# Performance work log

Hardware: AMD Instinct MI355X
Metric: run time of the kernel (lower is better)

Reference implementation:

```python
import jax, jax.numpy as jnp
import numpy as np

N = 4096
INPUT_DIM = 256
HIDDEN = 64
HEADS = 8
NEG_SLOPE = 0.2
MASK_FILL = -10000.0


def setup_inputs() -> dict:
    key = jax.random.key(0)
    k_x, k_adj, k_w, k_as, k_ad = jax.random.split(key, 5)
    x = jax.random.normal(k_x, (N, INPUT_DIM), dtype=jnp.float32)
    adjacency = jax.random.bernoulli(k_adj, 0.05, (N, N)) | jnp.eye(N, dtype=bool)
    # linear weight, torch convention: [out_features, in_features]
    W = jax.random.normal(k_w, (HEADS * HIDDEN, INPUT_DIM), dtype=jnp.float32) * 0.05
    attn_src = jax.random.normal(k_as, (HEADS, HIDDEN), dtype=jnp.float32) * 0.1
    attn_dst = jax.random.normal(k_ad, (HEADS, HIDDEN), dtype=jnp.float32) * 0.1
    return {"x": x, "adjacency": adjacency, "W": W, "attn_src": attn_src, "attn_dst": attn_dst}


def reference(x, adjacency, W, attn_src, attn_dst):
    # h: [N, heads, hidden]
    h = (x @ W.T).reshape(N, HEADS, HIDDEN)
    src_scores = jnp.einsum('nhd,hd->nh', h, attn_src)  # [N, heads]
    dst_scores = jnp.einsum('nhd,hd->nh', h, attn_dst)  # [N, heads]
    # logits[i, j, h] = src[i, h] + dst[j, h]  (matches torch permute(2,0,1) layout math)
    logits = src_scores[:, None, :] + dst_scores[None, :, :]  # [N, N, heads]
    logits = jax.nn.leaky_relu(logits, negative_slope=NEG_SLOPE)
    logits = jnp.where(adjacency[:, :, None], logits, MASK_FILL)
    alpha = jax.nn.softmax(logits, axis=1)  # softmax over source nodes j
    out = jnp.einsum('ijh,jhf->ihf', alpha, h)  # [N, heads, hidden]
    return out.mean(axis=1)  # [N, hidden]
```

## Files before the change

kernel.cpp:

```cpp
#include <hip/hip_runtime.h>

#define NN 4096
#define IN_DIM 256
#define HID 64
#define HEADS 8

typedef __attribute__((ext_vector_type(4))) float f32x4;
typedef __attribute__((ext_vector_type(8))) short s16x8;
typedef unsigned short u16;
typedef unsigned long long u64;

__device__ inline u16 f2bf(float f) {
  union { float f; unsigned u; } v; v.f = f;
  unsigned r = (v.u + 0x7FFFu + ((v.u >> 16) & 1u)) >> 16;
  return (u16)r;
}
__device__ inline float bf2f(u16 b) {
  union { unsigned u; float f; } v; v.u = ((unsigned)b) << 16;
  return v.f;
}
__device__ __forceinline__ unsigned cvt_pk_bf16(float a, float b) {
  unsigned r;
  asm("v_cvt_pk_bf16_f32 %0, %1, %2" : "=v"(r) : "v"(a), "v"(b));
  return r;
}
__device__ inline unsigned encf(float f) {
  unsigned u = __float_as_uint(f);
  return (u & 0x80000000u) ? ~u : (u | 0x80000000u);
}
__device__ inline float decf(unsigned k) {
  return (k & 0x80000000u) ? __uint_as_float(k & 0x7FFFFFFFu) : __uint_as_float(~k);
}

__global__ __launch_bounds__(256) void gat_prep(
    const void* __restrict__ adj, const float* __restrict__ x,
    const float* __restrict__ W, u64* __restrict__ bits,
    u16* __restrict__ xhi_g, u16* __restrict__ xlo_g,
    u16* __restrict__ whi_g, u16* __restrict__ wlo_g,
    unsigned* __restrict__ Mh_enc)
{
  const int t = threadIdx.x;
  const int gtid = blockIdx.x * 256 + t;
  if (blockIdx.x == 0 && t < 8) Mh_enc[t] = 0u;

  if (gtid < 262144) {
    f32x4 v = ((const f32x4*)x)[gtid];
    ushort4 hi, lo;
    hi.x = f2bf(v[0]); lo.x = f2bf(v[0] - bf2f(hi.x));
    hi.y = f2bf(v[1]); lo.y = f2bf(v[1] - bf2f(hi.y));
    hi.z = f2bf(v[2]); lo.z = f2bf(v[2] - bf2f(hi.z));
    hi.w = f2bf(v[3]); lo.w = f2bf(v[3] - bf2f(hi.w));
    ((ushort4*)xhi_g)[gtid] = hi;
    ((ushort4*)xlo_g)[gtid] = lo;
  }
  if (gtid < 32768) {
    f32x4 v = ((const f32x4*)W)[gtid];
    ushort4 hi, lo;
    hi.x = f2bf(v[0]); lo.x = f2bf(v[0] - bf2f(hi.x));
    hi.y = f2bf(v[1]); lo.y = f2bf(v[1] - bf2f(hi.y));
    hi.z = f2bf(v[2]); lo.z = f2bf(v[2] - bf2f(hi.z));
    hi.w = f2bf(v[3]); lo.w = f2bf(v[3] - bf2f(hi.w));
    ((ushort4*)whi_g)[gtid] = hi;
    ((ushort4*)wlo_g)[gtid] = lo;
  }

  __shared__ int smode;
  if (t < 64) {
    const unsigned char* a8 = (const unsigned char*)adj;
    const int* a32 = (const int*)adj;
    size_t i8 = (size_t)(4 * t + 1) * 4097;
    int p8 = a8[i8] != 0;
    size_t k = (size_t)(2 * t + 1);
    int p32 = a32[k * 4097] != 0;
    int p64 = a32[2 * k * 4097] != 0;
    int ok8 = __all(p8), ok32 = __all(p32), ok64 = __all(p64);
    if (t == 0) smode = ok8 ? 0 : (ok32 ? 1 : (ok64 ? 2 : 1));
  }
  __syncthreads();
  const int mode = smode;

  const int lane = t & 63;
  const int wave = (blockIdx.x * blockDim.x + t) >> 6;
  const int nwaves = (gridDim.x * blockDim.x) >> 6;
  const size_t nwords = (size_t)NN * NN / 64;
  for (size_t w = wave; w < nwords; w += nwaves) {
    size_t e = w * 64 + lane;
    int on;
    if (mode == 1)      on = ((const int*)adj)[e] != 0;
    else if (mode == 0) on = ((const unsigned char*)adj)[e] != 0;
    else                on = ((const long long*)adj)[e] != 0;
    u64 b = __ballot(on);
    if (lane == 0) bits[w] = b;
  }
}

__global__ __launch_bounds__(256) void gat_gemm1(
    const u16* __restrict__ xhi_g, const u16* __restrict__ xlo_g,
    const u16* __restrict__ whi_g, const u16* __restrict__ wlo_g,
    const float* __restrict__ a_src, const float* __restrict__ a_dst,
    u16* __restrict__ Hbt, float* __restrict__ s_srcT,
    float* __restrict__ s_dstT, unsigned* __restrict__ Mh_enc)
{
  __shared__ u16 xhi[64 * 72], xlo[64 * 72], whi[64 * 72], wlo[64 * 72];
  const int nb = blockIdx.x;
  const int ob = blockIdx.y;
  const int t = threadIdx.x;
  const int lane = t & 63, wid = t >> 6;
  const int wr = wid >> 1, wc = wid & 1;
  const int g = lane >> 4;

  f32x4 acc[2][2] = {};

  const int sn = t >> 2;
  const int skc = (t & 3) * 16;

  for (int kb = 0; kb < 4; ++kb) {
    const u16* xh_p = xhi_g + (size_t)(nb * 64 + sn) * IN_DIM + kb * 64 + skc;
    const u16* xl_p = xlo_g + (size_t)(nb * 64 + sn) * IN_DIM + kb * 64 + skc;
    const u16* wh_p = whi_g + (size_t)(ob * 64 + sn) * IN_DIM + kb * 64 + skc;
    const u16* wl_p = wlo_g + (size_t)(ob * 64 + sn) * IN_DIM + kb * 64 + skc;
    const int base = sn * 72 + skc;
    *(s16x8*)(xhi + base)     = *(const s16x8*)(xh_p);
    *(s16x8*)(xhi + base + 8) = *(const s16x8*)(xh_p + 8);
    *(s16x8*)(xlo + base)     = *(const s16x8*)(xl_p);
    *(s16x8*)(xlo + base + 8) = *(const s16x8*)(xl_p + 8);
    *(s16x8*)(whi + base)     = *(const s16x8*)(wh_p);
    *(s16x8*)(whi + base + 8) = *(const s16x8*)(wh_p + 8);
    *(s16x8*)(wlo + base)     = *(const s16x8*)(wl_p);
    *(s16x8*)(wlo + base + 8) = *(const s16x8*)(wl_p + 8);
    __syncthreads();
#pragma unroll
    for (int ks = 0; ks < 2; ++ks) {
      const int k0 = ks * 32 + g * 8;
      s16x8 ah[2], al[2], bh[2], bl[2];
#pragma unroll
      for (int nf = 0; nf < 2; ++nf) {
        int row = wr * 32 + nf * 16 + (lane & 15);
        ah[nf] = *(const s16x8*)(xhi + row * 72 + k0);
        al[nf] = *(const s16x8*)(xlo + row * 72 + k0);
      }
#pragma unroll
      for (int of = 0; of < 2; ++of) {
        int row = wc * 32 + of * 16 + (lane & 15);
        bh[of] = *(const s16x8*)(whi + row * 72 + k0);
        bl[of] = *(const s16x8*)(wlo + row * 72 + k0);
      }
#pragma unroll
      for (int nf = 0; nf < 2; ++nf)
#pragma unroll
        for (int of = 0; of < 2; ++of) {
          acc[nf][of] = __builtin_amdgcn_mfma_f32_16x16x32_bf16(ah[nf], bh[of], acc[nf][of], 0, 0, 0);
          acc[nf][of] = __builtin_amdgcn_mfma_f32_16x16x32_bf16(ah[nf], bl[of], acc[nf][of], 0, 0, 0);
          acc[nf][of] = __builtin_amdgcn_mfma_f32_16x16x32_bf16(al[nf], bh[of], acc[nf][of], 0, 0, 0);
        }
    }
    __syncthreads();
  }

  u16* Ct = xhi;
#pragma unroll
  for (int nf = 0; nf < 2; ++nf)
#pragma unroll
    for (int of = 0; of < 2; ++of)
#pragma unroll
      for (int r = 0; r < 4; ++r) {
        int nloc = wr * 32 + nf * 16 + g * 4 + r;
        int oloc = wc * 32 + of * 16 + (lane & 15);
        Ct[oloc * 72 + nloc] = f2bf(acc[nf][of][r]);
      }

  {
    const float* asp = a_src + ob * 64;
    const float* adp = a_dst + ob * 64;
    float as0 = asp[wc * 32 + (lane & 15)], as1 = asp[wc * 32 + 16 + (lane & 15)];
    float ad0 = adp[wc * 32 + (lane & 15)], ad1 = adp[wc * 32 + 16 + (lane & 15)];
    float* sred = (float*)wlo;
#pragma unroll
    for (int nf = 0; nf < 2; ++nf)
#pragma unroll
      for (int r = 0; r < 4; ++r) {
        float vs = acc[nf][0][r] * as0 + acc[nf][1][r] * as1;
        float vd = acc[nf][0][r] * ad0 + acc[nf][1][r] * ad1;
#pragma unroll
        for (int m = 1; m < 16; m <<= 1) { vs += __shfl_xor(vs, m); vd += __shfl_xor(vd, m); }
        if ((lane & 15) == 0) {
          int node = wr * 32 + nf * 16 + g * 4 + r;
          sred[wc * 64 + node] = vs;
          sred[128 + wc * 64 + node] = vd;
        }
      }
  }
  __syncthreads();
  {
    int o = t >> 2, nc = (t & 3) * 16;
    u16* dst = Hbt + ((size_t)(ob * 64 + nb) * 64 + o) * 64 + nc;
#pragma unroll
    for (int c = 0; c < 2; ++c) {
      s16x8 v = *(const s16x8*)(Ct + o * 72 + nc + c * 8);
      *(s16x8*)(dst + c * 8) = v;
    }
  }
  if (t < 64) {
    const float* sred = (const float*)wlo;
    float vssum = sred[t] + sred[64 + t];
    float vdsum = sred[128 + t] + sred[192 + t];
    s_srcT[(size_t)ob * NN + nb * 64 + t] = vssum;
    s_dstT[(size_t)ob * NN + nb * 64 + t] = vdsum;
    float m = vdsum;
#pragma unroll
    for (int s = 1; s < 64; s <<= 1) m = fmaxf(m, __shfl_xor(m, s));
    if (t == 0) atomicMax(Mh_enc + ob, encf(m));
  }
}

__global__ __launch_bounds__(512, 4) void gat_flash(
    const u64* __restrict__ bits, const u16* __restrict__ Hbt,
    const float* __restrict__ s_srcT, const float* __restrict__ s_dstT,
    const unsigned* __restrict__ Mh_enc, float* __restrict__ pout)
{
  __shared__ char shmem[32768];
  __shared__ float Lbuf[8][16];
  u16* Ast = (u16*)shmem;

  const int t = threadIdx.x, lane = t & 63, wid = t >> 6;
  const int ws4 = wid & 3, jh = wid >> 2;
  const int bid = blockIdx.x;
  const int h = bid & 7, iblk = bid >> 3;
  const int i_loc = lane & 15, g = lane >> 4, j0 = g * 8;
  const int irow = iblk * 64 + ws4 * 16 + i_loc;

  const float s_i = s_srcT[(size_t)h * NN + irow];
  float m_i = s_i + decf(Mh_enc[h]);
  m_i = fmaxf(m_i, 0.2f * m_i);
  const float L2E = 1.44269504f;
  const float mL = m_i * L2E;

  const u16* tile0 = Hbt + (size_t)h * 64 * 4096;
  const float* dT = s_dstT + (size_t)h * NN;

  const int lt = t & 255;
  const int r0 = lt >> 3, colE = (lt & 7) * 8;
  const int jtb = jh * 32;
  const u16* gsrc0 = tile0 + (size_t)jtb * 4096 + r0 * 64 + (colE ^ ((r0 & 7) << 3));
  const u16* gsrc1 = tile0 + (size_t)jtb * 4096 + (32 + r0) * 64 + (colE ^ ((r0 & 7) << 3));
  const u64* brow = bits + (size_t)irow * 64 + jtb;
  const float* dp = dT + jtb * 64 + j0;

  u16* sdstA = Ast + jh * 8192;
  u16* sdstB = sdstA + 4096;
  const char* lbaseA = (const char*)sdstA;
  const char* lbaseB = (const char*)sdstB;
  const int swz = (i_loc & 7) << 4;
  const int ofA0 = (g * 16) ^ swz, ofA1 = ((g * 16) + 64) ^ swz;

  s16x8 ones;
#pragma unroll
  for (int e = 0; e < 8; ++e) ones[e] = (short)0x3F80;

  f32x4 acc[4] = {};
  f32x4 acc_l = {0.f, 0.f, 0.f, 0.f};

#define QUAD(DV, MBITS, SH, PW0, PW1) do {                            \
    float z0 = s_i + DV[0], z1 = s_i + DV[1];                         \
    float z2 = s_i + DV[2], z3 = s_i + DV[3];                         \
    z0 = fmaxf(z0, 0.2f * z0); z1 = fmaxf(z1, 0.2f * z1);             \
    z2 = fmaxf(z2, 0.2f * z2); z3 = fmaxf(z3, 0.2f * z3);             \
    float e0 = __builtin_amdgcn_exp2f(__builtin_fmaf(z0, L2E, -mL));  \
    float e1 = __builtin_amdgcn_exp2f(__builtin_fmaf(z1, L2E, -mL));  \
    float e2 = __builtin_amdgcn_exp2f(__builtin_fmaf(z2, L2E, -mL));  \
    float e3 = __builtin_amdgcn_exp2f(__builtin_fmaf(z3, L2E, -mL));  \
    e0 = ((MBITS >> (SH + 0)) & 1u) ? e0 : 0.f;                       \
    e1 = ((MBITS >> (SH + 1)) & 1u) ? e1 : 0.f;                       \
    e2 = ((MBITS >> (SH + 2)) & 1u) ? e2 : 0.f;                       \
    e3 = ((MBITS >> (SH + 3)) & 1u) ? e3 : 0.f;                       \
    PW0 = cvt_pk_bf16(e0, e1); PW1 = cvt_pk_bf16(e2, e3);             \
  } while (0)

#define TILE_BODY(SDST, LBASE) do {                                   \
    *(s16x8*)((SDST) + lt * 8) = sv0;                                 \
    *(s16x8*)((SDST) + 2048 + lt * 8) = sv1;                          \
    gsrc0 += 4096; gsrc1 += 4096;                                     \
    sv0 = *(const s16x8*)(gsrc0);                                     \
    sv1 = *(const s16x8*)(gsrc1);                                     \
    const u64 am_ = *brow++;                                          \
    f32x4 d0 = *(const f32x4*)(dp);                                   \
    f32x4 d1 = *(const f32x4*)(dp + 4);                               \
    f32x4 d2 = *(const f32x4*)(dp + 32);                              \
    f32x4 d3 = *(const f32x4*)(dp + 36);                              \
    dp += 64;                                                         \
    const unsigned amlo = (unsigned)(am_ >> j0);                      \
    const unsigned amhi = (unsigned)(am_ >> (32 + j0));               \
    union { unsigned w_[4]; s16x8 v_; } P0, P1;                       \
    QUAD(d0, amlo, 0, P0.w_[0], P0.w_[1]);                            \
    QUAD(d1, amlo, 4, P0.w_[2], P0.w_[3]);                            \
    QUAD(d2, amhi, 0, P1.w_[0], P1.w_[1]);                            \
    QUAD(d3, amhi, 4, P1.w_[2], P1.w_[3]);                            \
    __syncthreads();                                                  \
    _Pragma("unroll")                                                 \
    for (int fb = 0; fb < 4; ++fb) {                                  \
      const int rowb = (fb * 16 + i_loc) * 128;                       \
      s16x8 A0 = *(const s16x8*)((LBASE) + rowb + ofA0);              \
      s16x8 A1 = *(const s16x8*)((LBASE) + rowb + ofA1);              \
      acc[fb] = __builtin_amdgcn_mfma_f32_16x16x32_bf16(A0, P0.v_, acc[fb], 0, 0, 0); \
      acc[fb] = __builtin_amdgcn_mfma_f32_16x16x32_bf16(A1, P1.v_, acc[fb], 0, 0, 0); \
    }                                                                 \
    acc_l = __builtin_amdgcn_mfma_f32_16x16x32_bf16(ones, P0.v_, acc_l, 0, 0, 0); \
    acc_l = __builtin_amdgcn_mfma_f32_16x16x32_bf16(ones, P1.v_, acc_l, 0, 0, 0); \
  } while (0)

  s16x8 sv0 = *(const s16x8*)(gsrc0);
  s16x8 sv1 = *(const s16x8*)(gsrc1);

  for (int it = 0; it < 16; ++it) {
    TILE_BODY(sdstA, lbaseA);
    TILE_BODY(sdstB, lbaseB);
  }
#undef QUAD
#undef TILE_BODY

  float l_run = acc_l[0];
  if (lane < 16) Lbuf[wid][i_loc] = l_run;

  __syncthreads();
  float* accst = (float*)shmem;
  if (jh == 1) {
    float* ab = accst + (ws4 * 16 + i_loc) * 66;
#pragma unroll
    for (int fb = 0; fb < 4; ++fb)
      *(f32x4*)(ab + fb * 16 + g * 4) = acc[fb];
  }
  __syncthreads();
  if (jh == 0) {
    const float invL = 1.f / (l_run + Lbuf[4 + ws4][i_loc]);
    float* ob = pout + ((size_t)h * NN + irow) * 64;
#pragma unroll
    for (int fb = 0; fb < 4; ++fb) {
      f32x4 v = acc[fb] +
          *(const f32x4*)(accst + (ws4 * 16 + i_loc) * 66 + fb * 16 + g * 4);
      *(f32x4*)(ob + fb * 16 + g * 4) = v * invL;
    }
  }
}

__global__ __launch_bounds__(256) void gat_combine(
    const float* __restrict__ pout, float* __restrict__ out)
{
  size_t e = (size_t)blockIdx.x * 256 + threadIdx.x;
  f32x4 s = {0.f, 0.f, 0.f, 0.f};
#pragma unroll
  for (int h = 0; h < 8; ++h)
    s += ((const f32x4*)pout)[(size_t)h * (NN * 16) + e];
  ((f32x4*)out)[e] = s * 0.125f;
}

extern "C" void kernel_launch(void* const* d_in, const int* in_sizes, int n_in,
                              void* d_out, int out_size, void* d_ws, size_t ws_size,
                              hipStream_t stream)
{
  const float* x = (const float*)d_in[0];
  const void* adj = d_in[1];
  const float* W = (const float*)d_in[2];
  const float* a_src = (const float*)d_in[3];
  const float* a_dst = (const float*)d_in[4];
  float* out = (float*)d_out;

  char* ws = (char*)d_ws;
  u16* xhi_g = (u16*)ws;
  u16* xlo_g = (u16*)(ws + 2 * 1024 * 1024);
  u16* whi_g = (u16*)(ws + 4 * 1024 * 1024);
  u16* wlo_g = (u16*)(ws + 4 * 1024 * 1024 + 256 * 1024);
  float* pout = (float*)ws;
  u16* Hbt = (u16*)(ws + 8 * 1024 * 1024);
  float* s_srcT = (float*)(ws + 12 * 1024 * 1024);
  float* s_dstT = (float*)(ws + 12 * 1024 * 1024 + 128 * 1024);
  unsigned* Mh_enc = (unsigned*)(ws + 12 * 1024 * 1024 + 384 * 1024);
  u64* bits = (u64*)(ws + 12 * 1024 * 1024 + 512 * 1024);

  gat_prep<<<2048, 256, 0, stream>>>(adj, x, W, bits, xhi_g, xlo_g, whi_g, wlo_g, Mh_enc);
  gat_gemm1<<<dim3(64, 8), 256, 0, stream>>>(xhi_g, xlo_g, whi_g, wlo_g,
                                             a_src, a_dst, Hbt, s_srcT, s_dstT, Mh_enc);
  gat_flash<<<512, 512, 0, stream>>>(bits, Hbt, s_srcT, s_dstT, Mh_enc, pout);
  gat_combine<<<256, 256, 0, stream>>>(pout, out);
}
```

Before: 91.29 us.

## Fuse prep into GEMM kernel and fold head-combine into flash via counters

Merges the bf16 split conversion of x and W into the GEMM1 tile loads, and runs the adjacency bit-packing on extra blocks of the same launch so both proceed concurrently. The separate combine kernel is removed: the last of the eight head blocks for each row block, found through an atomic counter, averages the heads and writes the output. Launch overhead and the global round-trip through the hi/lo bf16 buffers go away. In exchange there is a memset launch, redundant per-tile conversions (each x tile is converted once per output block), and threadfence/atomic synchronization.

```diff
diff --git a/kernel.cpp b/kernel.cpp
--- a/kernel.cpp
+++ b/kernel.cpp
@@ -32,79 +32,50 @@
   return (k & 0x80000000u) ? __uint_as_float(k & 0x7FFFFFFFu) : __uint_as_float(~k);
 }
 
-__global__ __launch_bounds__(256) void gat_prep(
+__global__ __launch_bounds__(256) void gat_main(
     const void* __restrict__ adj, const float* __restrict__ x,
-    const float* __restrict__ W, u64* __restrict__ bits,
-    u16* __restrict__ xhi_g, u16* __restrict__ xlo_g,
-    u16* __restrict__ whi_g, u16* __restrict__ wlo_g,
-    unsigned* __restrict__ Mh_enc)
-{
-  const int t = threadIdx.x;
-  const int gtid = blockIdx.x * 256 + t;
-  if (blockIdx.x == 0 && t < 8) Mh_enc[t] = 0u;
-
-  if (gtid < 262144) {
-    f32x4 v = ((const f32x4*)x)[gtid];
-    ushort4 hi, lo;
-    hi.x = f2bf(v[0]); lo.x = f2bf(v[0] - bf2f(hi.x));
-    hi.y = f2bf(v[1]); lo.y = f2bf(v[1] - bf2f(hi.y));
-    hi.z = f2bf(v[2]); lo.z = f2bf(v[2] - bf2f(hi.z));
-    hi.w = f2bf(v[3]); lo.w = f2bf(v[3] - bf2f(hi.w));
-    ((ushort4*)xhi_g)[gtid] = hi;
-    ((ushort4*)xlo_g)[gtid] = lo;
-  }
-  if (gtid < 32768) {
-    f32x4 v = ((const f32x4*)W)[gtid];
-    ushort4 hi, lo;
-    hi.x = f2bf(v[0]); lo.x = f2bf(v[0] - bf2f(hi.x));
-    hi.y = f2bf(v[1]); lo.y = f2bf(v[1] - bf2f(hi.y));
-    hi.z = f2bf(v[2]); lo.z = f2bf(v[2] - bf2f(hi.z));
-    hi.w = f2bf(v[3]); lo.w = f2bf(v[3] - bf2f(hi.w));
-    ((ushort4*)whi_g)[gtid] = hi;
-    ((ushort4*)wlo_g)[gtid] = lo;
-  }
-
-  __shared__ int smode;
-  if (t < 64) {
-    const unsigned char* a8 = (const unsigned char*)adj;
-    const int* a32 = (const int*)adj;
-    size_t i8 = (size_t)(4 * t + 1) * 4097;
-    int p8 = a8[i8] != 0;
-    size_t k = (size_t)(2 * t + 1);
-    int p32 = a32[k * 4097] != 0;
-    int p64 = a32[2 * k * 4097] != 0;
-    int ok8 = __all(p8), ok32 = __all(p32), ok64 = __all(p64);
-    if (t == 0) smode = ok8 ? 0 : (ok32 ? 1 : (ok64 ? 2 : 1));
-  }
-  __syncthreads();
-  const int mode = smode;
-
-  const int lane = t & 63;
-  const int wave = (blockIdx.x * blockDim.x + t) >> 6;
-  const int nwaves = (gridDim.x * blockDim.x) >> 6;
-  const size_t nwords = (size_t)NN * NN / 64;
-  for (size_t w = wave; w < nwords; w += nwaves) {
-    size_t e = w * 64 + lane;
-    int on;
-    if (mode == 1)      on = ((const int*)adj)[e] != 0;
-    else if (mode == 0) on = ((const unsigned char*)adj)[e] != 0;
-    else                on = ((const long long*)adj)[e] != 0;
-    u64 b = __ballot(on);
-    if (lane == 0) bits[w] = b;
-  }
-}
-
-__global__ __launch_bounds__(256) void gat_gemm1(
-    const u16* __restrict__ xhi_g, const u16* __restrict__ xlo_g,
-    const u16* __restrict__ whi_g, const u16* __restrict__ wlo_g,
-    const float* __restrict__ a_src, const float* __restrict__ a_dst,
-    u16* __restrict__ Hbt, float* __restrict__ s_srcT,
-    float* __restrict__ s_dstT, unsigned* __restrict__ Mh_enc)
+    const float* __restrict__ W, const float* __restrict__ a_src,
+    const float* __restrict__ a_dst, u16* __restrict__ Hbt,
+    float* __restrict__ s_srcT, float* __restrict__ s_dstT,
+    unsigned* __restrict__ Mh_enc, u64* __restrict__ bits)
 {
   __shared__ u16 xhi[64 * 72], xlo[64 * 72], whi[64 * 72], wlo[64 * 72];
-  const int nb = blockIdx.x;
-  const int ob = blockIdx.y;
+  __shared__ int smode;
   const int t = threadIdx.x;
+  const int bid = blockIdx.x;
+
+  if (bid >= 512) {
+    if (t < 64) {
+      const unsigned char* a8 = (const unsigned char*)adj;
+      const int* a32 = (const int*)adj;
+      size_t i8 = (size_t)(4 * t + 1) * 4097;
+      int p8 = a8[i8] != 0;
+      size_t k = (size_t)(2 * t + 1);
+      int p32 = a32[k * 4097] != 0;
+      int p64 = a32[2 * k * 4097] != 0;
+      int ok8 = __all(p8), ok32 = __all(p32), ok64 = __all(p64);
+      if (t == 0) smode = ok8 ? 0 : (ok32 ? 1 : (ok64 ? 2 : 1));
+    }
+    __syncthreads();
+    const int mode = smode;
+    const int lane = t & 63;
+    const int wave = (bid - 512) * 4 + (t >> 6);
+    const int nwaves = 1536 * 4;
+    const size_t nwords = (size_t)NN * NN / 64;
+    for (size_t w = wave; w < nwords; w += nwaves) {
+      size_t e = w * 64 + lane;
+      int on;
+      if (mode == 1)      on = ((const int*)adj)[e] != 0;
+      else if (mode == 0) on = ((const unsigned char*)adj)[e] != 0;
+      else                on = ((const long long*)adj)[e] != 0;
+      u64 b = __ballot(on);
+      if (lane == 0) bits[w] = b;
+    }
+    return;
+  }
+
+  const int nb = bid & 63;
+  const int ob = bid >> 6;
   const int lane = t & 63, wid = t >> 6;
   const int wr = wid >> 1, wc = wid & 1;
   const int g = lane >> 4;
@@ -115,19 +86,26 @@
   const int skc = (t & 3) * 16;
 
   for (int kb = 0; kb < 4; ++kb) {
-    const u16* xh_p = xhi_g + (size_t)(nb * 64 + sn) * IN_DIM + kb * 64 + skc;
-    const u16* xl_p = xlo_g + (size_t)(nb * 64 + sn) * IN_DIM + kb * 64 + skc;
-    const u16* wh_p = whi_g + (size_t)(ob * 64 + sn) * IN_DIM + kb * 64 + skc;
-    const u16* wl_p = wlo_g + (size_t)(ob * 64 + sn) * IN_DIM + kb * 64 + skc;
-    const int base = sn * 72 + skc;
-    *(s16x8*)(xhi + base)     = *(const s16x8*)(xh_p);
-    *(s16x8*)(xhi + base + 8) = *(const s16x8*)(xh_p + 8);
-    *(s16x8*)(xlo + base)     = *(const s16x8*)(xl_p);
-    *(s16x8*)(xlo + base + 8) = *(const s16x8*)(xl_p + 8);
-    *(s16x8*)(whi + base)     = *(const s16x8*)(wh_p);
-    *(s16x8*)(whi + base + 8) = *(const s16x8*)(wh_p + 8);
-    *(s16x8*)(wlo + base)     = *(const s16x8*)(wl_p);
-    *(s16x8*)(wlo + base + 8) = *(const s16x8*)(wl_p + 8);
+    const float* xr = x + (size_t)(nb * 64 + sn) * IN_DIM + kb * 64 + skc;
+    const float* wr_p = W + (size_t)(ob * 64 + sn) * IN_DIM + kb * 64 + skc;
+#pragma unroll
+    for (int c = 0; c < 4; ++c) {
+      float4 xv = ((const float4*)xr)[c];
+      float4 wv = ((const float4*)wr_p)[c];
+      float xf[4] = {xv.x, xv.y, xv.z, xv.w};
+      float wf[4] = {wv.x, wv.y, wv.z, wv.w};
+      u16 xh[4], xl[4], wh[4], wl[4];
+#pragma unroll
+      for (int e = 0; e < 4; ++e) {
+        xh[e] = f2bf(xf[e]); xl[e] = f2bf(xf[e] - bf2f(xh[e]));
+        wh[e] = f2bf(wf[e]); wl[e] = f2bf(wf[e] - bf2f(wh[e]));
+      }
+      int base = sn * 72 + skc + c * 4;
+      *(ushort4*)(xhi + base) = make_ushort4(xh[0], xh[1], xh[2], xh[3]);
+      *(ushort4*)(xlo + base) = make_ushort4(xl[0], xl[1], xl[2], xl[3]);
+      *(ushort4*)(whi + base) = make_ushort4(wh[0], wh[1], wh[2], wh[3]);
+      *(ushort4*)(wlo + base) = make_ushort4(wl[0], wl[1], wl[2], wl[3]);
+    }
     __syncthreads();
 #pragma unroll
     for (int ks = 0; ks < 2; ++ks) {
@@ -216,10 +194,12 @@
 __global__ __launch_bounds__(512, 4) void gat_flash(
     const u64* __restrict__ bits, const u16* __restrict__ Hbt,
     const float* __restrict__ s_srcT, const float* __restrict__ s_dstT,
-    const unsigned* __restrict__ Mh_enc, float* __restrict__ pout)
+    const unsigned* __restrict__ Mh_enc, float* __restrict__ pout,
+    float* __restrict__ outp, int* __restrict__ cnt)
 {
   __shared__ char shmem[32768];
   __shared__ float Lbuf[8][16];
+  __shared__ int sdone;
   u16* Ast = (u16*)shmem;
 
   const int t = threadIdx.x, lane = t & 63, wid = t >> 6;
@@ -340,17 +320,27 @@
       *(f32x4*)(ob + fb * 16 + g * 4) = v * invL;
     }
   }
-}
-
-__global__ __launch_bounds__(256) void gat_combine(
-    const float* __restrict__ pout, float* __restrict__ out)
-{
-  size_t e = (size_t)blockIdx.x * 256 + threadIdx.x;
-  f32x4 s = {0.f, 0.f, 0.f, 0.f};
-#pragma unroll
-  for (int h = 0; h < 8; ++h)
-    s += ((const f32x4*)pout)[(size_t)h * (NN * 16) + e];
-  ((f32x4*)out)[e] = s * 0.125f;
+
+  __syncthreads();
+  if (t == 0) {
+    __threadfence();
+    sdone = atomicAdd(cnt + iblk, 1);
+  }
+  __syncthreads();
+  if (sdone == 7) {
+    __threadfence();
+    const f32x4* p4 = (const f32x4*)pout;
+    f32x4* o4 = (f32x4*)outp;
+    const int base = iblk * 1024;
+#pragma unroll
+    for (int e = t; e < 1024; e += 512) {
+      f32x4 s = {0.f, 0.f, 0.f, 0.f};
+#pragma unroll
+      for (int hh = 0; hh < 8; ++hh)
+        s += p4[(size_t)hh * 65536 + base + e];
+      o4[base + e] = s * 0.125f;
+    }
+  }
 }
 
 extern "C" void kernel_launch(void* const* d_in, const int* in_sizes, int n_in,
@@ -365,20 +355,17 @@
   float* out = (float*)d_out;
 
   char* ws = (char*)d_ws;
-  u16* xhi_g = (u16*)ws;
-  u16* xlo_g = (u16*)(ws + 2 * 1024 * 1024);
-  u16* whi_g = (u16*)(ws + 4 * 1024 * 1024);
-  u16* wlo_g = (u16*)(ws + 4 * 1024 * 1024 + 256 * 1024);
   float* pout = (float*)ws;
   u16* Hbt = (u16*)(ws + 8 * 1024 * 1024);
   float* s_srcT = (float*)(ws + 12 * 1024 * 1024);
   float* s_dstT = (float*)(ws + 12 * 1024 * 1024 + 128 * 1024);
   unsigned* Mh_enc = (unsigned*)(ws + 12 * 1024 * 1024 + 384 * 1024);
+  int* cnt = (int*)(ws + 12 * 1024 * 1024 + 384 * 1024 + 32);
   u64* bits = (u64*)(ws + 12 * 1024 * 1024 + 512 * 1024);
 
-  gat_prep<<<2048, 256, 0, stream>>>(adj, x, W, bits, xhi_g, xlo_g, whi_g, wlo_g, Mh_enc);
-  gat_gemm1<<<dim3(64, 8), 256, 0, stream>>>(xhi_g, xlo_g, whi_g, wlo_g,
-                                             a_src, a_dst, Hbt, s_srcT, s_dstT, Mh_enc);
-  gat_flash<<<512, 512, 0, stream>>>(bits, Hbt, s_srcT, s_dstT, Mh_enc, pout);
-  gat_combine<<<256, 256, 0, stream>>>(pout, out);
-}
+  hipMemsetAsync(ws + 12 * 1024 * 1024 + 384 * 1024, 0, 288, stream);
+  gat_main<<<2048, 256, 0, stream>>>(adj, x, W, a_src, a_dst, Hbt,
+                                     s_srcT, s_dstT, Mh_enc, bits);
+  gat_flash<<<512, 512, 0, stream>>>(bits, Hbt, s_srcT, s_dstT, Mh_enc,
+                                     pout, out, cnt);
+}
```

Result: slower. 165.0 us (+80.8%).
